# Optimization experiments

Hardware: AMD Instinct MI355X
Metric: run time of the kernel (lower is better)

## Reference

```python
import jax, jax.numpy as jnp
import numpy as np
from jax import lax

NUM_ITER = 10
SMOOTH = 1.0
CL_WEIGHT = 0.5


def _min_pool(x, wh, ww):
    # torch: -max_pool2d(-x) pads with -inf -> min-pool with +inf boundary
    return lax.reduce_window(x, jnp.inf, lax.min,
                             (1, 1, wh, ww), (1, 1, 1, 1),
                             [(0, 0), (0, 0), (wh // 2, wh // 2), (ww // 2, ww // 2)])


def _max_pool(x, wh, ww):
    return lax.reduce_window(x, -jnp.inf, lax.max,
                             (1, 1, wh, ww), (1, 1, 1, 1),
                             [(0, 0), (0, 0), (wh // 2, wh // 2), (ww // 2, ww // 2)])


def soft_erode(img):
    return jnp.minimum(_min_pool(img, 3, 1), _min_pool(img, 1, 3))


def soft_dilate(img):
    return _max_pool(img, 3, 3)


def soft_open(img):
    return soft_dilate(soft_erode(img))


def soft_skeleton(img, num_iter=NUM_ITER):
    # img: (B,1,H,W)
    skel = jax.nn.relu(img - soft_open(img))

    def body(i, carry):
        img_e, skel = carry
        img_e = soft_erode(img_e)
        delta = jax.nn.relu(img_e - soft_open(img_e))
        skel = skel + jax.nn.relu(delta - skel * delta)
        return (img_e, skel)

    _, skel = lax.fori_loop(0, num_iter, body, (img, skel))
    return skel


def soft_dice(pred, target, smooth=SMOOTH):
    inter = jnp.sum(pred * target)
    return (2.0 * inter + smooth) / (jnp.sum(pred) + jnp.sum(target) + smooth)


def setup_inputs() -> dict:
    key = jax.random.key(0)
    k1, k2 = jax.random.split(key)
    pred = jax.random.normal(k1, (8, 1, 1024, 1024), dtype=jnp.float32)
    target = jax.random.randint(k2, (8, 1, 1024, 1024), 0, 2, dtype=jnp.int32)
    return {"pred": pred, "target": target}


def reference(pred, target):
    pred_prob = jax.nn.sigmoid(pred)          # (B,1,H,W)
    target_f = target.astype(pred_prob.dtype)

    skel_pred = soft_skeleton(pred_prob)
    skel_target = soft_skeleton(target_f)

    tprec = (jnp.sum(skel_pred * target_f) + SMOOTH) / (jnp.sum(skel_pred) + SMOOTH)
    tsens = (jnp.sum(skel_target * pred_prob) + SMOOTH) / (jnp.sum(skel_target) + SMOOTH)
    cl_dice = 2.0 * tprec * tsens / (tprec + tsens + 1e-7)

    dice = soft_dice(pred_prob, target_f)
    combined = (1.0 - CL_WEIGHT) * dice + CL_WEIGHT * cl_dice
    loss = 1.0 - combined
    return loss
```

## Files before the change

### kernel.cpp

```cpp
#include <hip/hip_runtime.h>
#include <math.h>

#define IMG 1024
#define NXT 26
#define NYT 16

typedef _Float16 h2 __attribute__((ext_vector_type(2)));
union UH { unsigned u; h2 h; };
__device__ __forceinline__ h2 u2h(unsigned u){ UH x; x.u=u; return x.h; }
__device__ __forceinline__ unsigned h2u(h2 h){ UH x; x.h=h; return x.u; }
__device__ __forceinline__ h2 pmin(h2 a,h2 b){ return __builtin_elementwise_min(a,b); }
__device__ __forceinline__ h2 pmax(h2 a,h2 b){ return __builtin_elementwise_max(a,b); }
__device__ __forceinline__ h2 funnel(h2 hi_src,h2 lo_src){ return u2h((h2u(lo_src)>>16)|(h2u(hi_src)<<16)); }
__device__ __forceinline__ unsigned wshr(unsigned old_,unsigned src){
  return (unsigned)__builtin_amdgcn_update_dpp((int)old_,(int)src,0x138,0xF,0xF,false);
}
__device__ __forceinline__ unsigned wshl(unsigned old_,unsigned src){
  return (unsigned)__builtin_amdgcn_update_dpp((int)old_,(int)src,0x130,0xF,0xF,false);
}
__device__ __forceinline__ float sigmoidf(float x){ return 1.0f/(1.0f+__expf(-x)); }

template<bool BND>
__device__ __forceinline__ void wave_tile(const float* __restrict__ pb, const int* __restrict__ tb,
                                          int or0, int oc0, int lane, float (&s)[7]){
  const int c  = oc0 - 12 + lane;
  const bool cv = (unsigned)c < (unsigned)IMG;
  const int cc = BND ? (c<0?0:(c>IMG-1?IMG-1:c)) : c;
  int lo=0, hi=88;
  unsigned pm0=~0u, pm1=~0u, pm2=0x00FFFFFFu;
  if (BND){
    lo = (or0<0)? -or0 : 0;
    hi = (IMG-or0<88)? IMG-or0 : 88;
    unsigned m[3];
    #pragma unroll
    for (int w=0;w<3;++w){
      int l = lo-32*w; l=l<0?0:(l>32?32:l);
      int h = hi-32*w; h=h<0?0:(h>32?32:h);
      unsigned mm=0;
      if (h>l){ unsigned top=(h>=32)?~0u:((1u<<h)-1u); unsigned bot=(l<=0)?0u:((1u<<l)-1u); mm=top&~bot; }
      m[w]=mm;
    }
    unsigned cin = cv?0u:~0u;
    pm0=m[0]&~cin; pm1=m[1]&~cin; pm2=m[2]&~cin;
  }
  const h2 twos  = {(_Float16)2.0f,(_Float16)2.0f};
  const h2 zerov = {(_Float16)0.0f,(_Float16)0.0f};

  h2 A[44], Bv[44], skel[32];
  unsigned t0=0,t1=0,t2=0xFF000000u;
  #pragma unroll
  for (int k=0;k<44;++k){
    int r0=or0+2*k, r1=r0+1;
    int g0 = BND ? (r0<0?0:(r0>IMG-1?IMG-1:r0)) : r0;
    int g1 = BND ? (r1<0?0:(r1>IMG-1?IMG-1:r1)) : r1;
    float x0 = pb[(long)g0*IMG+cc];
    float x1 = pb[(long)g1*IMG+cc];
    int v0 = tb[(long)g0*IMG+cc];
    int v1 = tb[(long)g1*IMG+cc];
    h2 hh; hh.x=(_Float16)sigmoidf(x0); hh.y=(_Float16)sigmoidf(x1);
    if (BND){
      bool bad = (2*k < lo) || (2*k >= hi);
      hh = (bad || !cv) ? twos : hh;
    }
    A[k]=hh;
    unsigned add = ((unsigned)(v0!=0)<<((2*k)&31)) | ((unsigned)(v1!=0)<<((2*k+1)&31));
    if (k<16) t0|=add; else if (k<32) t1|=add; else t2|=add;
  }
  if (BND){ t0 |= ~pm0; t1 |= ~pm1; t2 |= ~pm2; }
  const unsigned q0=t0,q1=t1,q2=t2;
  unsigned sk0=0,sk1=0,sk2=0;
  #pragma unroll
  for (int i=0;i<32;++i) skel[i]=zerov;

  auto ESTEP = [&](h2 (&S)[44], h2 (&D)[44]){
    h2 pf = funnel(S[0], twos);
    #pragma unroll
    for (int k=0;k<44;++k){
      h2 mc = S[k];
      h2 mn = (k<43)? S[k+1] : twos;
      h2 su = pf;
      h2 sd = funnel(mn, mc);
      pf = sd;
      h2 v3 = pmin(pmin(su,sd), mc);
      h2 l3 = u2h(wshr(h2u(twos), h2u(mc)));
      h2 r3 = u2h(wshl(h2u(twos), h2u(mc)));
      D[k] = pmin(pmin(l3,r3), v3);
    }
  };
  auto TSTEP = [&](){
    unsigned o0=t0,o1=t1,o2=t2;
    unsigned U0=(t0<<1)|1u,       U1=(t1<<1)|(t0>>31), U2=(t2<<1)|(t1>>31);
    unsigned D0=(t0>>1)|(t1<<31), D1=(t1>>1)|(t2<<31), D2=(t2>>1)|0x80000000u;
    unsigned L0=wshr(~0u,t0), L1=wshr(~0u,t1), L2=wshr(~0u,t2);
    unsigned R0=wshl(~0u,t0), R1=wshl(~0u,t1), R2=wshl(~0u,t2);
    t0 &= U0&D0&L0&R0; t1 &= U1&D1&L1&R1; t2 &= U2&D2&L2&R2;
    unsigned g0=t0, g1=t1, g2=t2;
    if (BND){ g0&=pm0; g1&=pm1; g2&=pm2; }
    unsigned V0 = g0|(g0<<1)|((g0>>1)|(g1<<31));
    unsigned V1 = g1|((g1<<1)|(g0>>31))|((g1>>1)|(g2<<31));
    unsigned V2 = g2|((g2<<1)|(g1>>31))|(g2>>1);
    unsigned d0 = V0|wshr(0u,V0)|wshl(0u,V0);
    unsigned d1 = V1|wshr(0u,V1)|wshl(0u,V1);
    unsigned d2 = V2|wshr(0u,V2)|wshl(0u,V2);
    sk0 |= o0&~d0; sk1 |= o1&~d1; sk2 |= o2&~d2;
  };
  auto PD = [&](h2 (&S)[44], h2 (&D)[44]){
    auto get = [&](int k)->h2{
      h2 x = D[k];
      if (BND){
        bool bad = (2*k < lo) || (2*k >= hi);
        x = (bad || !cv) ? zerov : x;
      }
      return x;
    };
    h2 dc = get(6);
    h2 pf = funnel(dc, get(5));
    #pragma unroll
    for (int k=6;k<38;++k){
      h2 dn = get(k+1);
      h2 fU = pf;
      h2 fD = funnel(dn, dc);
      pf = fD;
      h2 vm = pmax(pmax(fU,fD), dc);
      h2 lm = u2h(wshr(0u, h2u(vm)));
      h2 rr = u2h(wshl(0u, h2u(vm)));
      h2 hm = pmax(pmax(lm,rr), vm);
      h2 d  = pmax(S[k]-hm, zerov);
      h2 x2 = d - skel[k-6]*d;
      skel[k-6] = skel[k-6] + pmax(x2, zerov);
      dc = dn;
    }
  };
  auto STEP = [&](h2 (&S)[44], h2 (&D)[44]){
    ESTEP(S,D);
    TSTEP();
    PD(S,D);
  };
  #pragma unroll
  for (int p=0;p<5;++p){ STEP(A,Bv); STEP(Bv,A); }
  STEP(A,Bv);

  #pragma unroll
  for (int k2=0;k2<7;++k2) s[k2]=0.f;
  #pragma unroll
  for (int i=0;i<32;++i){
    int k=i+6;
    long r0 = (long)(or0+2*k);
    float x0 = pb[r0*IMG+cc], x1 = pb[(r0+1)*IMG+cc];
    float p0 = sigmoidf(x0), p1 = sigmoidf(x1);
    int b=(2*k)&31, w=(2*k)>>5;
    unsigned qw = (w==0)?q0:((w==1)?q1:q2);
    unsigned sw = (w==0)?sk0:((w==1)?sk1:sk2);
    float a0=(float)skel[i].x, a1=(float)skel[i].y;
    float tb0=(float)((qw>>b)&1u), tb1=(float)((qw>>(b+1))&1u);
    float sb0=(float)((sw>>b)&1u), sb1=(float)((sw>>(b+1))&1u);
    s[0]+=a0+a1;          s[1]+=a0*tb0+a1*tb1;
    s[2]+=sb0+sb1;        s[3]+=sb0*p0+sb1*p1;
    s[4]+=p0*tb0+p1*tb1;  s[5]+=p0+p1;  s[6]+=tb0+tb1;
  }
}

__global__ __launch_bounds__(128,1)
void cl_dice_main(const float* __restrict__ pred, const int* __restrict__ targ,
                  float* __restrict__ ws){
  __shared__ float red[2][8];
  const int tid=threadIdx.x, lane=tid&63, wv=tid>>6;
  const int wid = blockIdx.x*2 + wv;
  const int tx = wid % NXT; const int tt = wid/NXT;
  const int ty = tt % NYT;  const int z  = tt/NYT;
  const long base = (long)z*IMG*IMG;
  const int or0 = ty*64-12, oc0 = tx*40;
  const bool bnd = (tx==0)|(tx==NXT-1)|(ty==0)|(ty==NYT-1);
  float s[7];
  if (!bnd) wave_tile<false>(pred+base, targ+base, or0, oc0, lane, s);
  else      wave_tile<true >(pred+base, targ+base, or0, oc0, lane, s);
  const int c = oc0-12+lane;
  const float msk = ((lane>=12)&&(lane<=51)&&(c<IMG)) ? 1.f : 0.f;
  #pragma unroll
  for (int k=0;k<7;++k){
    float v = s[k]*msk;
    v+=__shfl_down(v,32); v+=__shfl_down(v,16); v+=__shfl_down(v,8);
    v+=__shfl_down(v,4);  v+=__shfl_down(v,2);  v+=__shfl_down(v,1);
    if (lane==0) red[wv][k]=v;
  }
  __syncthreads();
  if (tid<7) ws[blockIdx.x*8+tid] = red[0][tid]+red[1][tid];
}

__global__ __launch_bounds__(256)
void cl_dice_finalize(const float* __restrict__ ws, float* __restrict__ out, int nblk) {
  __shared__ float red[4][8];
  int tid = threadIdx.x;
  float acc[7] = {0,0,0,0,0,0,0};
  for (int i=tid; i<nblk; i+=256) {
    #pragma unroll
    for (int k=0;k<7;++k) acc[k] += ws[i*8 + k];
  }
  #pragma unroll
  for (int k=0;k<7;++k){
    float v = acc[k];
    v += __shfl_down(v,32); v += __shfl_down(v,16); v += __shfl_down(v,8);
    v += __shfl_down(v,4);  v += __shfl_down(v,2);  v += __shfl_down(v,1);
    if ((tid & 63) == 0) red[tid>>6][k] = v;
  }
  __syncthreads();
  if (tid == 0) {
    float t0[7];
    #pragma unroll
    for (int k=0;k<7;++k) t0[k] = red[0][k] + red[1][k] + red[2][k] + red[3][k];
    float sum_sp = t0[0], sum_spt = t0[1], sum_st = t0[2], sum_stp = t0[3];
    float inter  = t0[4], sum_p   = t0[5], sum_t  = t0[6];
    float tprec = (sum_spt + 1.0f) / (sum_sp + 1.0f);
    float tsens = (sum_stp + 1.0f) / (sum_st + 1.0f);
    float cl    = 2.0f * tprec * tsens / (tprec + tsens + 1e-7f);
    float dice  = (2.0f * inter + 1.0f) / (sum_p + sum_t + 1.0f);
    out[0] = 1.0f - 0.5f * (dice + cl);
  }
}

extern "C" void kernel_launch(void* const* d_in, const int* in_sizes, int n_in,
                              void* d_out, int out_size, void* d_ws, size_t ws_size,
                              hipStream_t stream) {
  const float* pred = (const float*)d_in[0];
  const int*   targ = (const int*)d_in[1];
  float* ws  = (float*)d_ws;
  float* out = (float*)d_out;

  const int B = in_sizes[0] / (IMG * IMG);
  const int nw   = NXT*NYT*B;
  const int nblk = nw / 2;
  cl_dice_main<<<nblk, 128, 0, stream>>>(pred, targ, ws);
  cl_dice_finalize<<<1, 256, 0, stream>>>(ws, out, nblk);
}
```

Before: 262.2 us.

## Fuse erode and dilate passes into one streaming loop with in-place buffer

New measurement: 366.7 us. +39.9%, slower.

```diff
diff --git a/kernel.cpp b/kernel.cpp
--- a/kernel.cpp
+++ b/kernel.cpp
@@ -46,7 +46,7 @@
   const h2 twos  = {(_Float16)2.0f,(_Float16)2.0f};
   const h2 zerov = {(_Float16)0.0f,(_Float16)0.0f};
 
-  h2 A[44], Bv[44], skel[32];
+  h2 S[44], skel[32];
   unsigned t0=0,t1=0,t2=0xFF000000u;
   #pragma unroll
   for (int k=0;k<44;++k){
@@ -62,7 +62,7 @@
       bool bad = (2*k < lo) || (2*k >= hi);
       hh = (bad || !cv) ? twos : hh;
     }
-    A[k]=hh;
+    S[k]=hh;
     unsigned add = ((unsigned)(v0!=0)<<((2*k)&31)) | ((unsigned)(v1!=0)<<((2*k+1)&31));
     if (k<16) t0|=add; else if (k<32) t1|=add; else t2|=add;
   }
@@ -72,73 +72,63 @@
   #pragma unroll
   for (int i=0;i<32;++i) skel[i]=zerov;
 
-  auto ESTEP = [&](h2 (&S)[44], h2 (&D)[44]){
-    h2 pf = funnel(S[0], twos);
-    #pragma unroll
-    for (int k=0;k<44;++k){
-      h2 mc = S[k];
-      h2 mn = (k<43)? S[k+1] : twos;
-      h2 su = pf;
-      h2 sd = funnel(mn, mc);
-      pf = sd;
-      h2 v3 = pmin(pmin(su,sd), mc);
-      h2 l3 = u2h(wshr(h2u(twos), h2u(mc)));
-      h2 r3 = u2h(wshl(h2u(twos), h2u(mc)));
-      D[k] = pmin(pmin(l3,r3), v3);
-    }
-  };
-  auto TSTEP = [&](){
-    unsigned o0=t0,o1=t1,o2=t2;
-    unsigned U0=(t0<<1)|1u,       U1=(t1<<1)|(t0>>31), U2=(t2<<1)|(t1>>31);
-    unsigned D0=(t0>>1)|(t1<<31), D1=(t1>>1)|(t2<<31), D2=(t2>>1)|0x80000000u;
-    unsigned L0=wshr(~0u,t0), L1=wshr(~0u,t1), L2=wshr(~0u,t2);
-    unsigned R0=wshl(~0u,t0), R1=wshl(~0u,t1), R2=wshl(~0u,t2);
-    t0 &= U0&D0&L0&R0; t1 &= U1&D1&L1&R1; t2 &= U2&D2&L2&R2;
-    unsigned g0=t0, g1=t1, g2=t2;
-    if (BND){ g0&=pm0; g1&=pm1; g2&=pm2; }
-    unsigned V0 = g0|(g0<<1)|((g0>>1)|(g1<<31));
-    unsigned V1 = g1|((g1<<1)|(g0>>31))|((g1>>1)|(g2<<31));
-    unsigned V2 = g2|((g2<<1)|(g1>>31))|(g2>>1);
-    unsigned d0 = V0|wshr(0u,V0)|wshl(0u,V0);
-    unsigned d1 = V1|wshr(0u,V1)|wshl(0u,V1);
-    unsigned d2 = V2|wshr(0u,V2)|wshl(0u,V2);
-    sk0 |= o0&~d0; sk1 |= o1&~d1; sk2 |= o2&~d2;
-  };
-  auto PD = [&](h2 (&S)[44], h2 (&D)[44]){
-    auto get = [&](int k)->h2{
-      h2 x = D[k];
-      if (BND){
-        bool bad = (2*k < lo) || (2*k >= hi);
-        x = (bad || !cv) ? zerov : x;
+  #pragma unroll 1
+  for (int j=0;j<11;++j){
+    {
+      unsigned o0=t0,o1=t1,o2=t2;
+      unsigned U0=(t0<<1)|1u,       U1=(t1<<1)|(t0>>31), U2=(t2<<1)|(t1>>31);
+      unsigned D0=(t0>>1)|(t1<<31), D1=(t1>>1)|(t2<<31), D2=(t2>>1)|0x80000000u;
+      unsigned L0=wshr(~0u,t0), L1=wshr(~0u,t1), L2=wshr(~0u,t2);
+      unsigned R0=wshl(~0u,t0), R1=wshl(~0u,t1), R2=wshl(~0u,t2);
+      t0 &= U0&D0&L0&R0; t1 &= U1&D1&L1&R1; t2 &= U2&D2&L2&R2;
+      unsigned g0=t0, g1=t1, g2=t2;
+      if (BND){ g0&=pm0; g1&=pm1; g2&=pm2; }
+      unsigned V0 = g0|(g0<<1)|((g0>>1)|(g1<<31));
+      unsigned V1 = g1|((g1<<1)|(g0>>31))|((g1>>1)|(g2<<31));
+      unsigned V2 = g2|((g2<<1)|(g1>>31))|(g2>>1);
+      unsigned d0 = V0|wshr(0u,V0)|wshl(0u,V0);
+      unsigned d1 = V1|wshr(0u,V1)|wshl(0u,V1);
+      unsigned d2 = V2|wshr(0u,V2)|wshl(0u,V2);
+      sk0 |= o0&~d0; sk1 |= o1&~d1; sk2 |= o2&~d2;
+    }
+    {
+      h2 pf = funnel(S[0], twos);
+      h2 est1 = zerov;
+      h2 dm1  = zerov;
+      h2 fprev= zerov;
+      #pragma unroll
+      for (int k=0;k<44;++k){
+        h2 mc = S[k];
+        h2 mn = (k<43)? S[k+1] : twos;
+        h2 sd = funnel(mn, mc);
+        h2 v3 = pmin(pmin(pf,sd), mc);
+        pf = sd;
+        h2 l3 = u2h(wshr(h2u(twos), h2u(mc)));
+        h2 r3 = u2h(wshl(h2u(twos), h2u(mc)));
+        h2 ek = pmin(pmin(l3,r3), v3);
+        h2 ekm = ek;
+        if (BND){
+          bool bad = (2*k < lo) || (2*k >= hi);
+          ekm = (bad || !cv) ? zerov : ek;
+        }
+        h2 fcur = zerov;
+        if (k>=6) fcur = funnel(ekm, dm1);
+        if (k>=7 && k<=38){
+          const int p = k-1;
+          h2 vm = pmax(pmax(fprev,fcur), dm1);
+          h2 lm = u2h(wshr(0u, h2u(vm)));
+          h2 rr = u2h(wshl(0u, h2u(vm)));
+          h2 hm = pmax(pmax(lm,rr), vm);
+          h2 d  = pmax(S[p]-hm, zerov);
+          h2 x2 = d - skel[p-6]*d;
+          skel[p-6] = skel[p-6] + pmax(x2, zerov);
+        }
+        if (k>=1) S[k-1] = est1;
+        est1 = ek; dm1 = ekm; fprev = fcur;
       }
-      return x;
-    };
-    h2 dc = get(6);
-    h2 pf = funnel(dc, get(5));
-    #pragma unroll
-    for (int k=6;k<38;++k){
-      h2 dn = get(k+1);
-      h2 fU = pf;
-      h2 fD = funnel(dn, dc);
-      pf = fD;
-      h2 vm = pmax(pmax(fU,fD), dc);
-      h2 lm = u2h(wshr(0u, h2u(vm)));
-      h2 rr = u2h(wshl(0u, h2u(vm)));
-      h2 hm = pmax(pmax(lm,rr), vm);
-      h2 d  = pmax(S[k]-hm, zerov);
-      h2 x2 = d - skel[k-6]*d;
-      skel[k-6] = skel[k-6] + pmax(x2, zerov);
-      dc = dn;
-    }
-  };
-  auto STEP = [&](h2 (&S)[44], h2 (&D)[44]){
-    ESTEP(S,D);
-    TSTEP();
-    PD(S,D);
-  };
-  #pragma unroll
-  for (int p=0;p<5;++p){ STEP(A,Bv); STEP(Bv,A); }
-  STEP(A,Bv);
+      S[43] = est1;
+    }
+  }
 
   #pragma unroll
   for (int k2=0;k2<7;++k2) s[k2]=0.f;
@@ -160,7 +150,7 @@
   }
 }
 
-__global__ __launch_bounds__(128,1)
+__global__ __launch_bounds__(128,8)
 void cl_dice_main(const float* __restrict__ pred, const int* __restrict__ targ,
                   float* __restrict__ ws){
   __shared__ float red[2][8];
```
